# Performance work log

Hardware: AMD Instinct MI355X
Metric: run time of the kernel (lower is better)

The kernel has to match this reference:

```python
import jax, jax.numpy as jnp
import numpy as np

B = 8          # events
P = 16384      # points per event (P > MAX_TOKENS -> selection path)
FEAT = 6
TOK = 768
MT = 128       # max_tokens
K = 16         # k_neighbors
IH = 256       # importance_hidden_dim
LN_EPS = 1e-5


def _linear_init(key, fan_in, fan_out):
    kw, kb = jax.random.split(key)
    lim = 1.0 / np.sqrt(fan_in)
    w = jax.random.uniform(kw, (fan_in, fan_out), jnp.float32, -lim, lim)
    b = jax.random.uniform(kb, (fan_out,), jnp.float32, -lim, lim)
    return w, b


def setup_inputs() -> dict:
    key = jax.random.key(0)
    ks = jax.random.split(key, 16)
    # point data: col0 = batch index (sorted, equal counts), cols1:5 = x,y,z,t
    xyzt = jax.random.normal(ks[0], (B * P, 4), jnp.float32)
    bidx = jnp.repeat(jnp.arange(B, dtype=jnp.float32), P)[:, None]
    coordinates = jnp.concatenate([bidx, xyzt], axis=-1)
    features = jax.random.normal(ks[1], (B * P, FEAT), jnp.float32)
    # gumbel noise = -log(-log(U+1e-10)+1e-10)
    u = jax.random.uniform(ks[2], (B, P), jnp.float32)
    gumbel_noise = -jnp.log(-jnp.log(u + 1e-10) + 1e-10)
    # feature MLP: 6->256->512->768 (ReLU) -> 768
    w1, b1 = _linear_init(ks[3], FEAT, 256)
    w2, b2 = _linear_init(ks[4], 256, 512)
    w3, b3 = _linear_init(ks[5], 512, 768)
    w4, b4 = _linear_init(ks[6], 768, TOK)
    # importance encoder: (768+4)->256, ReLU, LN, 256->256, ReLU, 256->1
    iw1, ib1 = _linear_init(ks[7], TOK + 4, IH)
    ln_g = jnp.ones((IH,), jnp.float32)
    ln_b = jnp.zeros((IH,), jnp.float32)
    iw2, ib2 = _linear_init(ks[8], IH, IH)
    iw3, ib3 = _linear_init(ks[9], IH, 1)
    # neighborhood MLP: 768->768, ReLU, 768->768
    nw1, nb1 = _linear_init(ks[10], TOK, TOK)
    nw2, nb2 = _linear_init(ks[11], TOK, TOK)
    log_temperature = jnp.zeros((), jnp.float32)  # log(1.0)
    return dict(coordinates=coordinates, features=features,
                log_temperature=log_temperature,
                w1=w1, b1=b1, w2=w2, b2=b2, w3=w3, b3=b3, w4=w4, b4=b4,
                iw1=iw1, ib1=ib1, ln_g=ln_g, ln_b=ln_b, iw2=iw2, ib2=ib2,
                iw3=iw3, ib3=ib3, nw1=nw1, nb1=nb1, nw2=nw2, nb2=nb2,
                gumbel_noise=gumbel_noise, batch_size=B)


def _forward(coordinates, features, log_temperature,
             w1, b1, w2, b2, w3, b3, w4, b4,
             iw1, ib1, ln_g, ln_b, iw2, ib2, iw3, ib3,
             nw1, nb1, nw2, nb2, gumbel_noise, batch_size):
    N = coordinates.shape[0]
    Pn = N // batch_size
    coords4 = coordinates[:, 1:5]  # [N,4] (x,y,z,t)
    # point feature MLP
    h = jax.nn.relu(features @ w1 + b1)
    h = jax.nn.relu(h @ w2 + b2)
    h = jax.nn.relu(h @ w3 + b3)
    pf = h @ w4 + b4  # [N, TOK]
    # importance scores (context-aware)
    z = jax.nn.relu(jnp.concatenate([pf, coords4], axis=-1) @ iw1 + ib1)
    mu = jnp.mean(z, axis=-1, keepdims=True)
    var = jnp.var(z, axis=-1, keepdims=True)
    z = (z - mu) / jnp.sqrt(var + LN_EPS) * ln_g + ln_b
    z = jax.nn.relu(z @ iw2 + ib2)
    imp = (z @ iw3 + ib3)[:, 0]  # [N]
    temp = jnp.maximum(jnp.exp(log_temperature), 0.1)
    # equal-count sorted batches -> reshape and vmap over events
    pf_b = pf.reshape(batch_size, Pn, TOK)
    c_b = coords4.reshape(batch_size, Pn, 4)
    imp_b = imp.reshape(batch_size, Pn)

    def per_event(feats, coords, scores, noise):
        # gumbel-softmax top-k selection (soft mode: weights unused downstream)
        pert = (scores + noise) / temp
        _, sel = jax.lax.top_k(pert, MT)            # [MT]
        cent = coords[sel]                           # [MT,4]
        # squared euclidean distances centroids -> all points (same KNN order as cdist)
        d2 = jnp.sum((cent[:, None, :] - coords[None, :, :]) ** 2, axis=-1)  # [MT,P]
        _, knn = jax.lax.top_k(-d2, K)               # [MT,K]
        nbr = feats[knn]                             # [MT,K,TOK]
        pooled = jnp.max(nbr, axis=1)                # [MT,TOK]
        tok = jax.nn.relu(pooled @ nw1 + nb1) @ nw2 + nb2
        order = jnp.argsort(cent[:, 3])              # sort tokens by time
        return tok[order], cent[order]

    tokens, cents = jax.vmap(per_event)(pf_b, c_b, imp_b, gumbel_noise)
    return tokens, cents


def reference(coordinates, features, log_temperature,
              w1, b1, w2, b2, w3, b3, w4, b4,
              iw1, ib1, ln_g, ln_b, iw2, ib2, iw3, ib3,
              nw1, nb1, nw2, nb2, gumbel_noise, batch_size):
    tokens, cents = _forward(coordinates, features, log_temperature,
                             w1, b1, w2, b2, w3, b3, w4, b4,
                             iw1, ib1, ln_g, ln_b, iw2, ib2, iw3, ib3,
                             nw1, nb1, nw2, nb2, gumbel_noise, batch_size)
    masks = jnp.ones((batch_size, MT), dtype=bool)  # all events have > MT points
    return tokens, cents, masks
```

## Files before the change

kernel.cpp:

```cpp
#include <hip/hip_runtime.h>
#include <hip/hip_bf16.h>

#define NPT   131072
#define BATCH 8
#define PPE   16384
#define MT    128
#define KNN   16
#define TOKD  768
#define ZSPLIT 4

typedef short bf16x8 __attribute__((ext_vector_type(8)));
typedef float f32x4  __attribute__((ext_vector_type(4)));

#define GL16(g, l) __builtin_amdgcn_global_load_lds(                         \
    (const __attribute__((address_space(1))) void*)(g),                      \
    (__attribute__((address_space(3))) void*)(l), 16, 0, 0)

__device__ __forceinline__ unsigned pack_hi(unsigned u0, unsigned u1) {
    return (u0 >> 16) | (u1 & 0xFFFF0000u);
}
__device__ __forceinline__ void split1(float x, short& h, short& l) {
    const unsigned u = __float_as_uint(x);
    h = (short)(u >> 16);
    const float r = x - __uint_as_float(u & 0xFFFF0000u);
    l = (short)(__float_as_uint(r) >> 16);
}

__global__ __launch_bounds__(256) void prep_kernel(const float* __restrict__ coords,
                                                   float4* __restrict__ c4f)
{
    const int i = blockIdx.x * 256 + threadIdx.x;
    if (i < NPT) {
        const long b = (long)i * 5;
        c4f[i] = make_float4(coords[b + 1], coords[b + 2], coords[b + 3], coords[b + 4]);
    }
}

__global__ __launch_bounds__(256) void wsplit_all(
    const float* __restrict__ w2, const float* __restrict__ w3,
    const float* __restrict__ w4, const float* __restrict__ iw2,
    const float* __restrict__ nw1, const float* __restrict__ nw2,
    short* w2h, short* w2l, short* w3h, short* w3l,
    short* w4h, short* w4l, short* i2h, short* i2l,
    short* n1h, short* n1l, short* n2h, short* n2l)
{
    const int b = blockIdx.x;
    const float* W; int K, N, Kpad, n; short *hi, *lo;
    if (b < 512)       { W = w2;  K = 256; N = 512; Kpad = 256; hi = w2h; lo = w2l; n = b; }
    else if (b < 1280) { W = w3;  K = 512; N = 768; Kpad = 512; hi = w3h; lo = w3l; n = b - 512; }
    else if (b < 2048) { W = w4;  K = 768; N = 768; Kpad = 768; hi = w4h; lo = w4l; n = b - 1280; }
    else if (b < 2304) { W = iw2; K = 256; N = 256; Kpad = 256; hi = i2h; lo = i2l; n = b - 2048; }
    else if (b < 3072) { W = nw1; K = 768; N = 768; Kpad = 768; hi = n1h; lo = n1l; n = b - 2304; }
    else               { W = nw2; K = 768; N = 768; Kpad = 768; hi = n2h; lo = n2l; n = b - 3072; }
    for (int k = threadIdx.x; k < Kpad; k += 256) {
        short h = 0, l = 0;
        if (k < K) split1(W[(long)k * N + n], h, l);
        hi[(long)n * Kpad + k] = h;
        lo[(long)n * Kpad + k] = l;
    }
}

__global__ __launch_bounds__(256) void w45_kernel(const float* __restrict__ w4,
                                                  const float* __restrict__ iw1,
                                                  const float* __restrict__ b4,
                                                  const float* __restrict__ ib1,
                                                  short* __restrict__ hi,
                                                  short* __restrict__ lo,
                                                  float* __restrict__ bias45)
{
    const int k = blockIdx.x, n = threadIdx.x;
    if (k < 768) {
        const float* wr = w4 + (long)k * 768;
        float v0 = 0.f, v1 = 0.f, v2 = 0.f, v3 = 0.f;
        for (int j = 0; j < 768; j += 4) {
            v0 += wr[j]     * iw1[(long)j * 256 + n];
            v1 += wr[j + 1] * iw1[(long)(j + 1) * 256 + n];
            v2 += wr[j + 2] * iw1[(long)(j + 2) * 256 + n];
            v3 += wr[j + 3] * iw1[(long)(j + 3) * 256 + n];
        }
        const float v = (v0 + v1) + (v2 + v3);
        short h, l; split1(v, h, l);
        hi[(long)n * 800 + k] = h;
        lo[(long)n * 800 + k] = l;
    } else if (k < 800) {
        const float v = (k < 772) ? iw1[(long)k * 256 + n] : 0.f;
        short h, l; split1(v, h, l);
        hi[(long)n * 800 + k] = h;
        lo[(long)n * 800 + k] = l;
    } else {
        float v0 = 0.f, v1 = 0.f, v2 = 0.f, v3 = 0.f;
        for (int j = 0; j < 768; j += 4) {
            v0 += b4[j]     * iw1[(long)j * 256 + n];
            v1 += b4[j + 1] * iw1[(long)(j + 1) * 256 + n];
            v2 += b4[j + 2] * iw1[(long)(j + 2) * 256 + n];
            v3 += b4[j + 3] * iw1[(long)(j + 3) * 256 + n];
        }
        bias45[n] = (v0 + v1) + (v2 + v3) + ib1[n];
    }
}

__global__ __launch_bounds__(256) void l1_kernel(const float* __restrict__ f,
                                                 const float* __restrict__ w1,
                                                 const float* __restrict__ b1,
                                                 short* __restrict__ hp,
                                                 short* __restrict__ lp,
                                                 int base,
                                                 const int* __restrict__ gather)
{
    const int r0 = blockIdx.x << 6, tid = threadIdx.x;
    float wc[6];
#pragma unroll
    for (int k = 0; k < 6; ++k) wc[k] = w1[k * 256 + tid];
    const float bb = b1[tid];
    for (int i = 0; i < 64; ++i) {
        const int r = r0 + i;
        int row = gather ? gather[r] : (base + r);
        row = (row < 0) ? 0 : ((row >= NPT) ? (NPT - 1) : row);
        float acc = bb;
#pragma unroll
        for (int k = 0; k < 6; ++k) acc += f[(long)row * 6 + k] * wc[k];
        acc = fmaxf(acc, 0.f);
        short h, l; split1(acc, h, l);
        hp[(long)r * 256 + tid] = h;
        lp[(long)r * 256 + tid] = l;
    }
}

__global__ __launch_bounds__(256) void gather_h3_kernel(const short* __restrict__ H3,
                                                        const int* __restrict__ knn_idx,
                                                        int off,
                                                        short* __restrict__ G)
{
    const int i = blockIdx.x;
    const int row = knn_idx[off + i];
    const int4* src = (const int4*)(H3 + (long)row * 768);
    int4* dst = (int4*)(G + (long)i * 768);
    if (threadIdx.x < 96) dst[threadIdx.x] = src[threadIdx.x];
}

__global__ __launch_bounds__(256, 3) void gemm_mf(
    const short* __restrict__ Aph, const short* __restrict__ Apl,
    const float* __restrict__ Afp, int Kpad,
    const short* __restrict__ Wth, const short* __restrict__ Wtl,
    const float* __restrict__ bias,
    short* __restrict__ Cph, short* __restrict__ Cpl, int KpadOut,
    float* __restrict__ Cf, short* __restrict__ Cp768,
    float* __restrict__ Cpool,
    const float* __restrict__ CoordC, int cfBase,
    int N, int relu, long partStride)
{
    __shared__ short Ah[128 * 32];
    __shared__ short Al[128 * 32];
    __shared__ short Bh[128 * 32];
    __shared__ short Bl[128 * 32];
    const int tid = threadIdx.x;
    int rowb, colb;
    {
        const int ncol = gridDim.x, nrow = gridDim.y;
        if ((nrow & 7) == 0) {
            const int id  = blockIdx.y * ncol + blockIdx.x;
            const int sgs = ncol << 3;
            const int sg = id / sgs, wi = id % sgs;
            rowb = (sg << 3) + (wi & 7);
            colb = wi >> 3;
        } else { rowb = blockIdx.y; colb = blockIdx.x; }
    }
    const int row0 = rowb << 7, col0 = colb << 7;
    const int wave = tid >> 6, lane = tid & 63;
    const int wr = wave >> 1, wc = wave & 1;
    const int q = lane >> 4, l16 = lane & 15;
    const int l2 = lane >> 2;
    const int ksw = (((lane & 3) ^ ((lane >> 3) & 3)) << 3);
    const int rchunk = ((q ^ ((l16 >> 1) & 3)) << 3);

    f32x4 acc[4][4];
#pragma unroll
    for (int mt = 0; mt < 4; ++mt)
#pragma unroll
        for (int nt = 0; nt < 4; ++nt)
            acc[mt][nt] = (f32x4){0.f, 0.f, 0.f, 0.f};

    const bool useAl = (Apl != nullptr) || (Aph == nullptr);
    const int nkT = Kpad >> 5;
    const int Z = gridDim.z, zb = blockIdx.z;
    const int t0 = (nkT * zb) / Z, t1 = (nkT * (zb + 1)) / Z;

    auto stage = [&](int t) {
        const int k0 = t << 5;
#pragma unroll
        for (int i = 0; i < 2; ++i) {
            const int mb = (wave << 5) + (i << 4);
            const long gb = (long)(col0 + mb + l2) * Kpad + k0 + ksw;
            GL16(&Wth[gb], &Bh[mb * 32]);
            GL16(&Wtl[gb], &Bl[mb * 32]);
        }
        if (Aph) {
#pragma unroll
            for (int i = 0; i < 2; ++i) {
                const int mb = (wave << 5) + (i << 4);
                const long ga = (long)(row0 + mb + l2) * Kpad + k0 + ksw;
                GL16(&Aph[ga], &Ah[mb * 32]);
                if (Apl) GL16(&Apl[ga], &Al[mb * 32]);
            }
        } else {
#pragma unroll
            for (int s = 0; s < 4; ++s) {
                const int l  = (s << 8) + tid;
                const int m  = l >> 3;
                const int k4 = (l & 7) << 2;
                const float4 v = *(const float4*)&Afp[(long)(row0 + m) * Kpad + k0 + k4];
                const unsigned u0 = __float_as_uint(v.x), u1 = __float_as_uint(v.y);
                const unsigned u2 = __float_as_uint(v.z), u3 = __float_as_uint(v.w);
                const unsigned r0 = __float_as_uint(v.x - __uint_as_float(u0 & 0xFFFF0000u));
                const unsigned r1 = __float_as_uint(v.y - __uint_as_float(u1 & 0xFFFF0000u));
                const unsigned r2 = __float_as_uint(v.z - __uint_as_float(u2 & 0xFFFF0000u));
                const unsigned r3 = __float_as_uint(v.w - __uint_as_float(u3 & 0xFFFF0000u));
                const int off = m * 32 + ((((k4 >> 3) ^ ((m >> 1) & 3)) << 3) | (k4 & 4));
                *(int2*)&Ah[off] = make_int2((int)pack_hi(u0, u1), (int)pack_hi(u2, u3));
                *(int2*)&Al[off] = make_int2((int)pack_hi(r0, r1), (int)pack_hi(r2, r3));
            }
        }
    };

    stage(t0);
    __syncthreads();

    for (int t = t0; t < t1; ++t) {
        bf16x8 ah[4], al[4], bh[4], bl[4];
#pragma unroll
        for (int i = 0; i < 4; ++i) {
            const int mrow = (wr << 6) + (i << 4) + l16;
            const int ncol = (wc << 6) + (i << 4) + l16;
            ah[i] = *(const bf16x8*)&Ah[mrow * 32 + rchunk];
            if (useAl) al[i] = *(const bf16x8*)&Al[mrow * 32 + rchunk];
            bh[i] = *(const bf16x8*)&Bh[ncol * 32 + rchunk];
            bl[i] = *(const bf16x8*)&Bl[ncol * 32 + rchunk];
        }
        __syncthreads();
        if (t + 1 < t1) stage(t + 1);
#pragma unroll
        for (int nt = 0; nt < 4; ++nt)
#pragma unroll
            for (int mt = 0; mt < 4; ++mt) {
                acc[mt][nt] = __builtin_amdgcn_mfma_f32_16x16x32_bf16(ah[mt], bh[nt], acc[mt][nt], 0, 0, 0);
                acc[mt][nt] = __builtin_amdgcn_mfma_f32_16x16x32_bf16(ah[mt], bl[nt], acc[mt][nt], 0, 0, 0);
                if (useAl)
                    acc[mt][nt] = __builtin_amdgcn_mfma_f32_16x16x32_bf16(al[mt], bh[nt], acc[mt][nt], 0, 0, 0);
            }
        __syncthreads();
    }

    if (Cf && Z > 1) {
        float* dst = Cf + (long)zb * partStride;
#pragma unroll
        for (int mt = 0; mt < 4; ++mt)
#pragma unroll
            for (int nt = 0; nt < 4; ++nt) {
                const int col = col0 + (wc << 6) + (nt << 4) + l16;
#pragma unroll
                for (int rg = 0; rg < 4; ++rg) {
                    const int row = row0 + (wr << 6) + (mt << 4) + (q << 2) + rg;
                    dst[(long)row * N + col] = acc[mt][nt][rg];
                }
            }
        return;
    }

    if (Cpool) {
#pragma unroll
        for (int mt = 0; mt < 4; ++mt)
#pragma unroll
            for (int nt = 0; nt < 4; ++nt) {
                const int col = col0 + (wc << 6) + (nt << 4) + l16;
                float m = fmaxf(fmaxf(acc[mt][nt][0], acc[mt][nt][1]),
                                fmaxf(acc[mt][nt][2], acc[mt][nt][3]));
                m = fmaxf(m, __shfl_xor(m, 16));
                m = fmaxf(m, __shfl_xor(m, 32));
                m += bias[col];
                if (relu) m = fmaxf(m, 0.f);
                if (q == 0)
                    Cpool[(long)((row0 >> 4) + (wr << 2) + mt) * 768 + col] = m;
            }
        return;
    }
#pragma unroll
    for (int mt = 0; mt < 4; ++mt)
#pragma unroll
        for (int nt = 0; nt < 4; ++nt) {
            const int col = col0 + (wc << 6) + (nt << 4) + l16;
            const float bs = bias[col];
#pragma unroll
            for (int rg = 0; rg < 4; ++rg) {
                const int row = row0 + (wr << 6) + (mt << 4) + (q << 2) + rg;
                float v = acc[mt][nt][rg] + bs;
                if (relu) v = fmaxf(v, 0.f);
                if (Cf) Cf[(long)row * N + col] = v;
                if (Cph || Cp768) {
                    short h, l; split1(v, h, l);
                    if (Cph) {
                        Cph[(long)row * KpadOut + col] = h;
                        Cpl[(long)row * KpadOut + col] = l;
                    }
                    if (Cp768) Cp768[(long)row * 768 + col] = h;
                }
            }
        }
    if (CoordC && Cph && colb == 0 && tid < 128) {
        const int r = row0 + tid;
        const long rb = (long)r * KpadOut;
        const long cb = (long)(cfBase + r) * 5;
#pragma unroll
        for (int d = 0; d < 4; ++d) {
            short h, l; split1(CoordC[cb + 1 + d], h, l);
            Cph[rb + 768 + d] = h;
            Cpl[rb + 768 + d] = l;
        }
        for (int c = 772; c < 800; ++c) { Cph[rb + c] = 0; Cpl[rb + c] = 0; }
    }
}

__global__ __launch_bounds__(256) void ln_kernel(const float* __restrict__ Fp,
                                                 long pstride,
                                                 const float* __restrict__ g,
                                                 const float* __restrict__ b,
                                                 const float* __restrict__ badd,
                                                 short* __restrict__ hp,
                                                 short* __restrict__ lp)
{
    const int tid = threadIdx.x, wave = tid >> 6, lane = tid & 63;
    float gv[4], bv[4], av[4];
#pragma unroll
    for (int j = 0; j < 4; ++j) {
        gv[j] = g[lane * 4 + j]; bv[j] = b[lane * 4 + j]; av[j] = badd[lane * 4 + j];
    }
    for (int i = 0; i < 2; ++i) {
        const int r = (blockIdx.x << 3) + (wave << 1) + i;
        const long off = (long)r * 256 + lane * 4;
        float4 x = *(const float4*)&Fp[off];
#pragma unroll
        for (int z = 1; z < ZSPLIT; ++z) {
            const float4 p = *(const float4*)&Fp[(long)z * pstride + off];
            x.x += p.x; x.y += p.y; x.z += p.z; x.w += p.w;
        }
        x.x = fmaxf(x.x + av[0], 0.f);
        x.y = fmaxf(x.y + av[1], 0.f);
        x.z = fmaxf(x.z + av[2], 0.f);
        x.w = fmaxf(x.w + av[3], 0.f);
        float s = x.x + x.y + x.z + x.w;
#pragma unroll
        for (int off2 = 32; off2; off2 >>= 1) s += __shfl_down(s, off2);
        const float mu = __shfl(s, 0) * (1.f / 256.f);
        const float d0 = x.x - mu, d1 = x.y - mu, d2 = x.z - mu, d3 = x.w - mu;
        float s2 = d0 * d0 + d1 * d1 + d2 * d2 + d3 * d3;
#pragma unroll
        for (int off2 = 32; off2; off2 >>= 1) s2 += __shfl_down(s2, off2);
        const float den = sqrtf(__shfl(s2, 0) * (1.f / 256.f) + 1e-5f);
        const float v[4] = { d0 / den * gv[0] + bv[0], d1 / den * gv[1] + bv[1],
                             d2 / den * gv[2] + bv[2], d3 / den * gv[3] + bv[3] };
#pragma unroll
        for (int j = 0; j < 4; ++j) {
            short h, l; split1(v[j], h, l);
            hp[(long)r * 256 + lane * 4 + j] = h;
            lp[(long)r * 256 + lane * 4 + j] = l;
        }
    }
}

__global__ __launch_bounds__(256) void imp_kernel(const float* __restrict__ Fp,
                                                  long pstride,
                                                  const float* __restrict__ iw3,
                                                  const float* __restrict__ ib3,
                                                  const float* __restrict__ ib2,
                                                  const float* __restrict__ noise,
                                                  const float* __restrict__ lt,
                                                  float* __restrict__ pert,
                                                  int base)
{
    const int tid = threadIdx.x, wave = tid >> 6, lane = tid & 63;
    float wv[4], bv[4];
#pragma unroll
    for (int j = 0; j < 4; ++j) { wv[j] = iw3[lane * 4 + j]; bv[j] = ib2[lane * 4 + j]; }
    const float temp = fmaxf(expf(lt[0]), 0.1f);
    const float b3v = ib3[0];
    for (int i = 0; i < 2; ++i) {
        const int r = (blockIdx.x << 3) + (wave << 1) + i;
        const long off = (long)r * 256 + lane * 4;
        float4 x = *(const float4*)&Fp[off];
#pragma unroll
        for (int z = 1; z < ZSPLIT; ++z) {
            const float4 p = *(const float4*)&Fp[(long)z * pstride + off];
            x.x += p.x; x.y += p.y; x.z += p.z; x.w += p.w;
        }
        float s = fmaxf(x.x + bv[0], 0.f) * wv[0] + fmaxf(x.y + bv[1], 0.f) * wv[1]
                + fmaxf(x.z + bv[2], 0.f) * wv[2] + fmaxf(x.w + bv[3], 0.f) * wv[3];
#pragma unroll
        for (int off2 = 32; off2; off2 >>= 1) s += __shfl_down(s, off2);
        if (lane == 0)
            pert[base + r] = (s + b3v + noise[base + r]) / temp;
    }
}

__device__ __forceinline__ unsigned fmap(float f) {
    unsigned x = __float_as_uint(f);
    return (x & 0x80000000u) ? ~x : (x | 0x80000000u);
}

__global__ __launch_bounds__(256) void topk_kernel(const float* __restrict__ pert,
                                                   const float4* __restrict__ c4f,
                                                   float* __restrict__ centf)
{
    const int e = blockIdx.x, tid = threadIdx.x;
    const int base = e * PPE;
    const int c4 = tid & 3;
    __shared__ unsigned short d16[PPE];
    __shared__ unsigned long long ubuf[664];
    __shared__ int sh_need; __shared__ unsigned sh_b;
    __shared__ int cgt, ceq;
    unsigned* hist4 = (unsigned*)ubuf;
    unsigned* histm = hist4 + 1024;
    for (int i = tid; i < 1024; i += 256) hist4[i] = 0;
    __syncthreads();
    for (int p = tid; p < PPE; p += 256) {
        const unsigned u = fmap(pert[base + p]);
        d16[p] = (unsigned short)(u >> 16);
        atomicAdd(&hist4[((u >> 24) << 2) | c4], 1u);
    }
    __syncthreads();
    histm[tid] = hist4[tid << 2] + hist4[(tid << 2) | 1]
               + hist4[(tid << 2) | 2] + hist4[(tid << 2) | 3];
    __syncthreads();
    if (tid == 0) {
        int cum = 0, b = 255;
        for (; b > 0; --b) { cum += (int)histm[b]; if (cum >= MT) break; }
        if (cum < MT) { cum += (int)histm[0]; b = 0; }
        sh_need = MT - (cum - (int)histm[b]); sh_b = (unsigned)b;
    }
    __syncthreads();
    int need = sh_need;
    const unsigned b1v = sh_b;
    __syncthreads();
    for (int i = tid; i < 1024; i += 256) hist4[i] = 0;
    __syncthreads();
    for (int p = tid; p < PPE; p += 256) {
        const unsigned h = d16[p];
        if ((h >> 8) == b1v) atomicAdd(&hist4[((h & 255u) << 2) | c4], 1u);
    }
    __syncthreads();
    histm[tid] = hist4[tid << 2] + hist4[(tid << 2) | 1]
               + hist4[(tid << 2) | 2] + hist4[(tid << 2) | 3];
    __syncthreads();
    if (tid == 0) {
        int cum = 0, b = 255;
        for (; b > 0; --b) { cum += (int)histm[b]; if (cum >= need) break; }
        if (cum < need) { cum += (int)histm[0]; b = 0; }
        sh_need = need - (cum - (int)histm[b]); sh_b = (unsigned)b;
    }
    __syncthreads();
    need = sh_need;
    const unsigned prefix16 = (b1v << 8) | sh_b;
    int* gt_i = (int*)ubuf;
    unsigned* gt_u = (unsigned*)(gt_i + MT);
    int* eqbuf = (int*)(gt_u + MT);
    unsigned long long* key256 = (unsigned long long*)(eqbuf + 256);
    unsigned long long* key = key256 + 256;
    if (tid == 0) { cgt = 0; ceq = 0; }
    __syncthreads();
    for (int p = tid; p < PPE; p += 256) {
        const unsigned h = d16[p];
        if (h > prefix16)        { int q = atomicAdd(&cgt, 1); if (q < MT)  gt_i[q] = p; }
        else if (h == prefix16)  { int q = atomicAdd(&ceq, 1); if (q < 256) eqbuf[q] = p; }
    }
    __syncthreads();
    const int ngt = (cgt < MT) ? cgt : MT;
    if (tid < ngt) gt_u[tid] = fmap(pert[base + gt_i[tid]]);
    if (ceq <= 256) {
        key256[tid] = (tid < ceq)
            ? (((unsigned long long)fmap(pert[base + eqbuf[tid]]) << 32) | (unsigned)(~eqbuf[tid]))
            : 0ull;
        __syncthreads();
        for (int k = 2; k <= 256; k <<= 1)
            for (int j = k >> 1; j > 0; j >>= 1) {
                const int l = tid ^ j;
                if (l > tid) {
                    const unsigned long long a = key256[tid], b = key256[l];
                    const bool up = ((tid & k) == 0);
                    if (up ? (a < b) : (a > b)) { key256[tid] = b; key256[l] = a; }
                }
                __syncthreads();
            }
    } else if (tid == 0) {
        unsigned long long sel[MT];
        int n = 0;
        for (int p = 0; p < PPE; ++p) {
            if (d16[p] != (unsigned short)prefix16) continue;
            const unsigned long long kk =
                ((unsigned long long)fmap(pert[base + p]) << 32) | (unsigned)(~p);
            if (n < need) {
                int j = n++;
                while (j > 0 && sel[j - 1] < kk) { sel[j] = sel[j - 1]; --j; }
                sel[j] = kk;
            } else if (kk > sel[need - 1]) {
                int j = need - 1;
                while (j > 0 && sel[j - 1] < kk) { sel[j] = sel[j - 1]; --j; }
                sel[j] = kk;
            }
        }
        for (int j = 0; j < need; ++j) key256[j] = sel[j];
    }
    __syncthreads();
    if (tid < MT) {
        if (tid < ngt)
            key[tid] = ((unsigned long long)gt_u[tid] << 32) | (unsigned)(~gt_i[tid]);
        else if (tid < ngt + need)
            key[tid] = key256[tid - ngt];
        else
            key[tid] = 0ull;
    }
    __syncthreads();
    for (int k = 2; k <= MT; k <<= 1)
        for (int j = k >> 1; j > 0; j >>= 1) {
            if (tid < MT) {
                const int l = tid ^ j;
                if (l > tid) {
                    const unsigned long long a = key[tid], b = key[l];
                    const bool up = ((tid & k) == 0);
                    if (up ? (a < b) : (a > b)) { key[tid] = b; key[l] = a; }
                }
            }
            __syncthreads();
        }
    if (tid < MT) {
        const int idx = (int)(~(unsigned)(key[tid] & 0xFFFFFFFFu));
        *(float4*)&centf[(long)(e * MT + tid) * 4] = c4f[base + idx];
    }
}

__device__ __forceinline__ unsigned d2bits(const float4 x, float c0, float c1,
                                           float c2, float c3) {
    const float q0 = __fmul_rn(c0 - x.x, c0 - x.x);
    const float q1 = __fmul_rn(c1 - x.y, c1 - x.y);
    const float q2 = __fmul_rn(c2 - x.z, c2 - x.z);
    const float q3 = __fmul_rn(c3 - x.w, c3 - x.w);
    return __float_as_uint(__fadd_rn(__fadd_rn(__fadd_rn(q0, q1), q2), q3));
}

__global__ __launch_bounds__(256) void knn_kernel(const float4* __restrict__ c4f,
                                                  const float* __restrict__ centf,
                                                  int* __restrict__ knn_idx)
{
    const int blk = blockIdx.x, tid = threadIdx.x;
    const int e = blk >> 7, base = e * PPE;
    const int c4 = tid & 3;
    const float c0 = centf[(long)blk * 4 + 0];
    const float c1 = centf[(long)blk * 4 + 1];
    const float c2 = centf[(long)blk * 4 + 2];
    const float c3 = centf[(long)blk * 4 + 3];
    __shared__ unsigned short d16[PPE];
    __shared__ unsigned long long ubuf[664];
    __shared__ int sh_need; __shared__ unsigned sh_b;
    __shared__ int clt, ceq;
    unsigned* hist4 = (unsigned*)ubuf;
    unsigned* histm = hist4 + 1024;
    for (int i = tid; i < 1024; i += 256) hist4[i] = 0;
    __syncthreads();
    for (int p = tid; p < PPE; p += 256) {
        const unsigned u = d2bits(c4f[base + p], c0, c1, c2, c3);
        d16[p] = (unsigned short)(u >> 16);
        atomicAdd(&hist4[((u >> 24) << 2) | c4], 1u);
    }
    __syncthreads();
    histm[tid] = hist4[tid << 2] + hist4[(tid << 2) | 1]
               + hist4[(tid << 2) | 2] + hist4[(tid << 2) | 3];
    __syncthreads();
    if (tid == 0) {
        int cum = 0, b = 0;
        for (; b < 255; ++b) { cum += (int)histm[b]; if (cum >= KNN) break; }
        if (cum < KNN) { cum += (int)histm[255]; b = 255; }
        sh_need = KNN - (cum - (int)histm[b]); sh_b = (unsigned)b;
    }
    __syncthreads();
    int need = sh_need;
    const unsigned b1v = sh_b;
    __syncthreads();
    for (int i = tid; i < 1024; i += 256) hist4[i] = 0;
    __syncthreads();
    for (int p = tid; p < PPE; p += 256) {
        const unsigned h = d16[p];
        if ((h >> 8) == b1v) atomicAdd(&hist4[((h & 255u) << 2) | c4], 1u);
    }
    __syncthreads();
    histm[tid] = hist4[tid << 2] + hist4[(tid << 2) | 1]
               + hist4[(tid << 2) | 2] + hist4[(tid << 2) | 3];
    __syncthreads();
    if (tid == 0) {
        int cum = 0, b = 0;
        for (; b < 255; ++b) { cum += (int)histm[b]; if (cum >= need) break; }
        if (cum < need) { cum += (int)histm[255]; b = 255; }
        sh_need = need - (cum - (int)histm[b]); sh_b = (unsigned)b;
    }
    __syncthreads();
    need = sh_need;
    const unsigned prefix16 = (b1v << 8) | sh_b;
    int* lt_i = (int*)ubuf;
    unsigned* lt_u = (unsigned*)(lt_i + KNN);
    int* eqbuf = (int*)(lt_u + KNN);
    unsigned long long* key256 = (unsigned long long*)(eqbuf + 256);
    if (tid == 0) { clt = 0; ceq = 0; }
    __syncthreads();
    for (int p = tid; p < PPE; p += 256) {
        const unsigned h = d16[p];
        if (h < prefix16)        { int q = atomicAdd(&clt, 1); if (q < KNN) lt_i[q] = p; }
        else if (h == prefix16)  { int q = atomicAdd(&ceq, 1); if (q < 256) eqbuf[q] = p; }
    }
    __syncthreads();
    const int nlt = (clt < KNN) ? clt : KNN;
    if (tid < nlt) lt_u[tid] = d2bits(c4f[base + lt_i[tid]], c0, c1, c2, c3);
    if (ceq <= 256) {
        key256[tid] = (tid < ceq)
            ? (((unsigned long long)d2bits(c4f[base + eqbuf[tid]], c0, c1, c2, c3) << 32)
               | (unsigned)eqbuf[tid])
            : 0xFFFFFFFFFFFFFFFFull;
        __syncthreads();
        for (int k = 2; k <= 256; k <<= 1)
            for (int j = k >> 1; j > 0; j >>= 1) {
                const int l = tid ^ j;
                if (l > tid) {
                    const unsigned long long a = key256[tid], b = key256[l];
                    const bool up = ((tid & k) == 0);
                    if (up ? (a > b) : (a < b)) { key256[tid] = b; key256[l] = a; }
                }
                __syncthreads();
            }
    } else if (tid == 0) {
        unsigned long long sel[KNN];
        int n = 0;
        for (int p = 0; p < PPE; ++p) {
            if (d16[p] != (unsigned short)prefix16) continue;
            const unsigned long long kk =
                ((unsigned long long)d2bits(c4f[base + p], c0, c1, c2, c3) << 32) | (unsigned)p;
            if (n < need) {
                int j = n++;
                while (j > 0 && sel[j - 1] > kk) { sel[j] = sel[j - 1]; --j; }
                sel[j] = kk;
            } else if (kk < sel[need - 1]) {
                int j = need - 1;
                while (j > 0 && sel[j - 1] > kk) { sel[j] = sel[j - 1]; --j; }
                sel[j] = kk;
            }
        }
        for (int j = 0; j < need; ++j) key256[j] = sel[j];
    }
    __syncthreads();
    if (tid == 0) {
        unsigned long long fin[KNN];
        int n = 0;
        for (int i = 0; i < nlt; ++i) {
            const unsigned long long kk = ((unsigned long long)lt_u[i] << 32) | (unsigned)lt_i[i];
            int j = n++;
            while (j > 0 && fin[j - 1] > kk) { fin[j] = fin[j - 1]; --j; }
            fin[j] = kk;
        }
        for (int i = 0; i < need; ++i) {
            const unsigned long long kk = key256[i];
            int j = n++;
            while (j > 0 && fin[j - 1] > kk) { fin[j] = fin[j - 1]; --j; }
            fin[j] = kk;
        }
        for (int r = 0; r < KNN; ++r)
            knn_idx[blk * KNN + r] = base + (int)(unsigned)(fin[r] & 0xFFFFFFFFu);
    }
}

__global__ __launch_bounds__(256) void emit_kernel(const float* __restrict__ centf,
                                                   const float* __restrict__ tokf,
                                                   float* __restrict__ out,
                                                   long out_size)
{
    const int e = blockIdx.x, s = blockIdx.y, tid = threadIdx.x;
    __shared__ float tv[MT];
    __shared__ int   rk[MT];
    if (tid < MT) tv[tid] = centf[(long)(e * MT + tid) * 4 + 3];
    __syncthreads();
    if (tid < MT) {
        const float t = tv[tid]; int r = 0;
        for (int j = 0; j < MT; ++j)
            r += (tv[j] < t || (tv[j] == t && j < tid)) ? 1 : 0;
        rk[tid] = r;
    }
    __syncthreads();
    const long cent_off = (long)BATCH * MT * TOKD;
    const long mask_off = cent_off + (long)BATCH * MT * 4;
    for (int i = s * 8; i < s * 8 + 8; ++i) {
        const float* src = tokf + ((size_t)e * MT + i) * TOKD;
        const long dst = ((long)e * MT + rk[i]) * TOKD;
        for (int t4 = tid; t4 < TOKD / 4; t4 += 256) {
            const float4 v = ((const float4*)src)[t4];
            const long g = dst + (long)t4 * 4;
            if (g + 3 < out_size) {
                *(float4*)&out[g] = v;
            } else {
                if (g + 0 < out_size) out[g + 0] = v.x;
                if (g + 1 < out_size) out[g + 1] = v.y;
                if (g + 2 < out_size) out[g + 2] = v.z;
                if (g + 3 < out_size) out[g + 3] = v.w;
            }
        }
    }
    if (s == 0) {
        for (int idx = tid; idx < MT * 4; idx += 256) {
            const int i = idx >> 2, d = idx & 3;
            const long g = cent_off + ((long)e * MT + rk[i]) * 4 + d;
            if (g < out_size) out[g] = centf[((long)e * MT + i) * 4 + d];
        }
        for (int idx = tid; idx < MT; idx += 256) {
            const long g = mask_off + (long)e * MT + idx;
            if (g < out_size) out[g] = 1.0f;
        }
    }
}

extern "C" void kernel_launch(void* const* d_in, const int* in_sizes, int n_in,
                              void* d_out, int out_size, void* d_ws, size_t ws_size,
                              hipStream_t stream)
{
    const float* coords = (const float*)d_in[0];
    const float* feats  = (const float*)d_in[1];
    const float* lt     = (const float*)d_in[2];
    const float* w1  = (const float*)d_in[3];  const float* b1  = (const float*)d_in[4];
    const float* w2  = (const float*)d_in[5];  const float* b2  = (const float*)d_in[6];
    const float* w3  = (const float*)d_in[7];  const float* b3  = (const float*)d_in[8];
    const float* w4  = (const float*)d_in[9];  const float* b4  = (const float*)d_in[10];
    const float* iw1 = (const float*)d_in[11]; const float* ib1 = (const float*)d_in[12];
    const float* lng = (const float*)d_in[13]; const float* lnb = (const float*)d_in[14];
    const float* iw2 = (const float*)d_in[15]; const float* ib2 = (const float*)d_in[16];
    const float* iw3 = (const float*)d_in[17]; const float* ib3 = (const float*)d_in[18];
    const float* nw1 = (const float*)d_in[19]; const float* nb1 = (const float*)d_in[20];
    const float* nw2 = (const float*)d_in[21]; const float* nb2 = (const float*)d_in[22];
    const float* noise = (const float*)d_in[23];

    const int NBR = BATCH * MT * KNN;
    const size_t FIXED_FL = (size_t)NPT + 4096 + 16384 + (size_t)1024 * TOKD
                          + (size_t)NPT * 4 + 256 + 2 * (size_t)1024 * TOKD;
    const size_t s_w2 = 512 * 256,  s_w3 = 768 * 512,  s_w4 = 768 * 768;
    const size_t s_45 = 256 * 800,  s_i2 = 256 * 256;
    const size_t s_n1 = 768 * 768,  s_n2 = 768 * 768;
    const size_t WTOT = 2 * (s_w2 + s_w3 + s_w4 + s_45 + s_i2 + s_n1 + s_n2);
    const size_t BASE_BYTES = FIXED_FL * 4 + WTOT * 2;
    const size_t PERROW = (800 * 2 + 512 * 2) * 2 + (size_t)ZSPLIT * 256 * 4;
    int ch = 128;
    while (ch < NPT && BASE_BYTES + (size_t)(ch * 2) * PERROW <= ws_size) ch <<= 1;
    const size_t H3_BYTES = (size_t)NPT * 768 * 2;
    const bool persist = (BASE_BYTES + (size_t)ch * PERROW + H3_BYTES) <= ws_size;

    float*  pert   = (float*)d_ws;
    float*  centf  = pert + NPT;
    int*    knn    = (int*)(centf + 4096);
    float*  pooled = (float*)(knn + 16384);
    float4* c4f    = (float4*)(pooled + (size_t)1024 * TOKD);
    float*  bias45 = (float*)(c4f + NPT);
    float*  T1     = bias45 + 256;
    float*  T2     = T1 + (size_t)1024 * TOKD;
    short*  wsp    = (short*)(T2 + (size_t)1024 * TOKD);
    short* w2h = wsp;            short* w2l = w2h + s_w2;
    short* w3h = w2l + s_w2;     short* w3l = w3h + s_w3;
    short* w4h = w3l + s_w3;     short* w4l = w4h + s_w4;
    short* f45h = w4l + s_w4;    short* f45l = f45h + s_45;
    short* i2h = f45l + s_45;    short* i2l = i2h + s_i2;
    short* n1h = i2l + s_i2;     short* n1l = n1h + s_n1;
    short* n2h = n1l + s_n1;     short* n2l = n2h + s_n2;
    short* PAh = n2l + s_n2;     short* PAl = PAh + (size_t)ch * 800;
    short* PBh = PAl + (size_t)ch * 800;
    short* PBl = PBh + (size_t)ch * 512;
    float* Fp  = (float*)(PBl + (size_t)ch * 512);
    short* H3  = (short*)(Fp + (size_t)ZSPLIT * ch * 256);
    const long pstride = (long)ch * 256;

    prep_kernel<<<dim3((NPT + 255) / 256), dim3(256), 0, stream>>>(coords, c4f);
    wsplit_all<<<dim3(3840), dim3(256), 0, stream>>>(
        w2, w3, w4, iw2, nw1, nw2,
        w2h, w2l, w3h, w3l, w4h, w4l, i2h, i2l, n1h, n1l, n2h, n2l);
    w45_kernel<<<dim3(801), dim3(256), 0, stream>>>(w4, iw1, b4, ib1, f45h, f45l, bias45);

    for (int ck = 0; ck < NPT / ch; ++ck) {
        const int base = ck * ch;
        l1_kernel<<<dim3(ch / 64), dim3(256), 0, stream>>>(feats, w1, b1, PAh, PAl, base, nullptr);
        gemm_mf<<<dim3(512 / 128, ch / 128), dim3(256), 0, stream>>>(
            PAh, PAl, nullptr, 256, w2h, w2l, b2, PBh, PBl, 512,
            nullptr, nullptr, nullptr, nullptr, 0, 512, 1, 0);
        gemm_mf<<<dim3(768 / 128, ch / 128), dim3(256), 0, stream>>>(
            PBh, PBl, nullptr, 512, w3h, w3l, b3, PAh, PAl, 800,
            nullptr, persist ? (H3 + (size_t)base * 768) : nullptr, nullptr,
            coords, base, 768, 1, 0);
        gemm_mf<<<dim3(256 / 128, ch / 128, ZSPLIT), dim3(256), 0, stream>>>(
            PAh, PAl, nullptr, 800, f45h, f45l, nullptr, nullptr, nullptr, 0,
            Fp, nullptr, nullptr, nullptr, 0, 256, 0, pstride);
        ln_kernel<<<dim3(ch / 8), dim3(256), 0, stream>>>(
            Fp, pstride, lng, lnb, bias45, PBh, PBl);
        gemm_mf<<<dim3(256 / 128, ch / 128, ZSPLIT), dim3(256), 0, stream>>>(
            PBh, PBl, nullptr, 256, i2h, i2l, nullptr, nullptr, nullptr, 0,
            Fp, nullptr, nullptr, nullptr, 0, 256, 0, pstride);
        imp_kernel<<<dim3(ch / 8), dim3(256), 0, stream>>>(
            Fp, pstride, iw3, ib3, ib2, noise, lt, pert, base);
    }

    topk_kernel<<<dim3(BATCH), dim3(256), 0, stream>>>(pert, c4f, centf);
    knn_kernel<<<dim3(BATCH * MT), dim3(256), 0, stream>>>(c4f, centf, knn);

    const int rcch = (ch < NBR) ? ch : NBR;
    for (int rc = 0; rc < NBR / rcch; ++rc) {
        if (persist) {
            gather_h3_kernel<<<dim3(rcch), dim3(256), 0, stream>>>(
                H3, knn, rc * rcch, PAh);
            gemm_mf<<<dim3(768 / 128, rcch / 128), dim3(256), 0, stream>>>(
                PAh, nullptr, nullptr, 768, w4h, w4l, b4, nullptr, nullptr, 0,
                nullptr, nullptr, pooled + (size_t)(rc * rcch / 16) * 768,
                nullptr, 0, 768, 0, 0);
        } else {
            l1_kernel<<<dim3(rcch / 64), dim3(256), 0, stream>>>(feats, w1, b1, PAh, PAl, 0, knn + (size_t)rc * rcch);
            gemm_mf<<<dim3(512 / 128, rcch / 128), dim3(256), 0, stream>>>(
                PAh, PAl, nullptr, 256, w2h, w2l, b2, PBh, PBl, 512,
                nullptr, nullptr, nullptr, nullptr, 0, 512, 1, 0);
            gemm_mf<<<dim3(768 / 128, rcch / 128), dim3(256), 0, stream>>>(
                PBh, PBl, nullptr, 512, w3h, w3l, b3, PAh, PAl, 768,
                nullptr, nullptr, nullptr, nullptr, 0, 768, 1, 0);
            gemm_mf<<<dim3(768 / 128, rcch / 128), dim3(256), 0, stream>>>(
                PAh, PAl, nullptr, 768, w4h, w4l, b4, nullptr, nullptr, 0,
                nullptr, nullptr, pooled + (size_t)(rc * rcch / 16) * 768,
                nullptr, 0, 768, 0, 0);
        }
    }

    gemm_mf<<<dim3(768 / 128, 1024 / 128), dim3(256), 0, stream>>>(
        nullptr, nullptr, pooled, 768, n1h, n1l, nb1, nullptr, nullptr, 0,
        T1, nullptr, nullptr, nullptr, 0, 768, 1, 0);
    gemm_mf<<<dim3(768 / 128, 1024 / 128), dim3(256), 0, stream>>>(
        nullptr, nullptr, T1, 768, n2h, n2l, nb2, nullptr, nullptr, 0,
        T2, nullptr, nullptr, nullptr, 0, 768, 0, 0);
    emit_kernel<<<dim3(BATCH, 16), dim3(256), 0, stream>>>(
        centf, T2, (float*)d_out, (long)out_size);
}
```

Measured before the change: 1.875 ms.

## Replace single-block radix top-k with two-stage bitonic partial sort and merge

The per-event radix-histogram top-k, which ran on only 8 blocks, is replaced by a two-stage scheme. 64 blocks each bitonic-sort a 2048-element slice and emit their top 128 candidates, then 8 merge blocks sort the 1024 candidates per event. This spreads the selection across more CUs at the cost of more sorting work, an extra launch and a candidate buffer. ZSPLIT also drops from 4 to 2, halving the split-K partial buffers and the reduction work in the LN and importance kernels in exchange for less parallelism in those GEMMs.

Result: faster. 1.673 ms (-10.8%).

```diff
diff --git a/kernel.cpp b/kernel.cpp
--- a/kernel.cpp
+++ b/kernel.cpp
@@ -7,7 +7,7 @@
 #define MT    128
 #define KNN   16
 #define TOKD  768
-#define ZSPLIT 4
+#define ZSPLIT 2
 
 typedef short bf16x8 __attribute__((ext_vector_type(8)));
 typedef float f32x4  __attribute__((ext_vector_type(4)));
@@ -405,133 +405,54 @@
     return (x & 0x80000000u) ? ~x : (x | 0x80000000u);
 }
 
-__global__ __launch_bounds__(256) void topk_kernel(const float* __restrict__ pert,
-                                                   const float4* __restrict__ c4f,
-                                                   float* __restrict__ centf)
+__global__ __launch_bounds__(256) void topk_part(const float* __restrict__ pert,
+                                                 unsigned long long* __restrict__ cand)
+{
+    const int e = blockIdx.x >> 3, s = blockIdx.x & 7, tid = threadIdx.x;
+    const int base = e * PPE + s * 2048;
+    __shared__ unsigned long long key[2048];
+    for (int i = tid; i < 2048; i += 256)
+        key[i] = ((unsigned long long)fmap(pert[base + i]) << 32) | (unsigned)(~(base + i));
+    __syncthreads();
+    for (int k = 2; k <= 2048; k <<= 1)
+        for (int j = k >> 1; j > 0; j >>= 1) {
+            for (int i = tid; i < 2048; i += 256) {
+                const int l = i ^ j;
+                if (l > i) {
+                    const unsigned long long a = key[i], b = key[l];
+                    const bool up = ((i & k) == 0);
+                    if (up ? (a < b) : (a > b)) { key[i] = b; key[l] = a; }
+                }
+            }
+            __syncthreads();
+        }
+    if (tid < MT) cand[(long)blockIdx.x * MT + tid] = key[tid];
+}
+
+__global__ __launch_bounds__(256) void topk_merge(const unsigned long long* __restrict__ cand,
+                                                  const float4* __restrict__ c4f,
+                                                  float* __restrict__ centf)
 {
     const int e = blockIdx.x, tid = threadIdx.x;
-    const int base = e * PPE;
-    const int c4 = tid & 3;
-    __shared__ unsigned short d16[PPE];
-    __shared__ unsigned long long ubuf[664];
-    __shared__ int sh_need; __shared__ unsigned sh_b;
-    __shared__ int cgt, ceq;
-    unsigned* hist4 = (unsigned*)ubuf;
-    unsigned* histm = hist4 + 1024;
-    for (int i = tid; i < 1024; i += 256) hist4[i] = 0;
-    __syncthreads();
-    for (int p = tid; p < PPE; p += 256) {
-        const unsigned u = fmap(pert[base + p]);
-        d16[p] = (unsigned short)(u >> 16);
-        atomicAdd(&hist4[((u >> 24) << 2) | c4], 1u);
-    }
-    __syncthreads();
-    histm[tid] = hist4[tid << 2] + hist4[(tid << 2) | 1]
-               + hist4[(tid << 2) | 2] + hist4[(tid << 2) | 3];
-    __syncthreads();
-    if (tid == 0) {
-        int cum = 0, b = 255;
-        for (; b > 0; --b) { cum += (int)histm[b]; if (cum >= MT) break; }
-        if (cum < MT) { cum += (int)histm[0]; b = 0; }
-        sh_need = MT - (cum - (int)histm[b]); sh_b = (unsigned)b;
-    }
-    __syncthreads();
-    int need = sh_need;
-    const unsigned b1v = sh_b;
-    __syncthreads();
-    for (int i = tid; i < 1024; i += 256) hist4[i] = 0;
-    __syncthreads();
-    for (int p = tid; p < PPE; p += 256) {
-        const unsigned h = d16[p];
-        if ((h >> 8) == b1v) atomicAdd(&hist4[((h & 255u) << 2) | c4], 1u);
-    }
-    __syncthreads();
-    histm[tid] = hist4[tid << 2] + hist4[(tid << 2) | 1]
-               + hist4[(tid << 2) | 2] + hist4[(tid << 2) | 3];
-    __syncthreads();
-    if (tid == 0) {
-        int cum = 0, b = 255;
-        for (; b > 0; --b) { cum += (int)histm[b]; if (cum >= need) break; }
-        if (cum < need) { cum += (int)histm[0]; b = 0; }
-        sh_need = need - (cum - (int)histm[b]); sh_b = (unsigned)b;
-    }
-    __syncthreads();
-    need = sh_need;
-    const unsigned prefix16 = (b1v << 8) | sh_b;
-    int* gt_i = (int*)ubuf;
-    unsigned* gt_u = (unsigned*)(gt_i + MT);
-    int* eqbuf = (int*)(gt_u + MT);
-    unsigned long long* key256 = (unsigned long long*)(eqbuf + 256);
-    unsigned long long* key = key256 + 256;
-    if (tid == 0) { cgt = 0; ceq = 0; }
-    __syncthreads();
-    for (int p = tid; p < PPE; p += 256) {
-        const unsigned h = d16[p];
-        if (h > prefix16)        { int q = atomicAdd(&cgt, 1); if (q < MT)  gt_i[q] = p; }
-        else if (h == prefix16)  { int q = atomicAdd(&ceq, 1); if (q < 256) eqbuf[q] = p; }
-    }
-    __syncthreads();
-    const int ngt = (cgt < MT) ? cgt : MT;
-    if (tid < ngt) gt_u[tid] = fmap(pert[base + gt_i[tid]]);
-    if (ceq <= 256) {
-        key256[tid] = (tid < ceq)
-            ? (((unsigned long long)fmap(pert[base + eqbuf[tid]]) << 32) | (unsigned)(~eqbuf[tid]))
-            : 0ull;
-        __syncthreads();
-        for (int k = 2; k <= 256; k <<= 1)
-            for (int j = k >> 1; j > 0; j >>= 1) {
-                const int l = tid ^ j;
-                if (l > tid) {
-                    const unsigned long long a = key256[tid], b = key256[l];
-                    const bool up = ((tid & k) == 0);
-                    if (up ? (a < b) : (a > b)) { key256[tid] = b; key256[l] = a; }
-                }
-                __syncthreads();
-            }
-    } else if (tid == 0) {
-        unsigned long long sel[MT];
-        int n = 0;
-        for (int p = 0; p < PPE; ++p) {
-            if (d16[p] != (unsigned short)prefix16) continue;
-            const unsigned long long kk =
-                ((unsigned long long)fmap(pert[base + p]) << 32) | (unsigned)(~p);
-            if (n < need) {
-                int j = n++;
-                while (j > 0 && sel[j - 1] < kk) { sel[j] = sel[j - 1]; --j; }
-                sel[j] = kk;
-            } else if (kk > sel[need - 1]) {
-                int j = need - 1;
-                while (j > 0 && sel[j - 1] < kk) { sel[j] = sel[j - 1]; --j; }
-                sel[j] = kk;
-            }
-        }
-        for (int j = 0; j < need; ++j) key256[j] = sel[j];
-    }
-    __syncthreads();
-    if (tid < MT) {
-        if (tid < ngt)
-            key[tid] = ((unsigned long long)gt_u[tid] << 32) | (unsigned)(~gt_i[tid]);
-        else if (tid < ngt + need)
-            key[tid] = key256[tid - ngt];
-        else
-            key[tid] = 0ull;
-    }
-    __syncthreads();
-    for (int k = 2; k <= MT; k <<= 1)
+    __shared__ unsigned long long key[1024];
+    for (int i = tid; i < 1024; i += 256)
+        key[i] = cand[(long)e * 1024 + i];
+    __syncthreads();
+    for (int k = 2; k <= 1024; k <<= 1)
         for (int j = k >> 1; j > 0; j >>= 1) {
-            if (tid < MT) {
-                const int l = tid ^ j;
-                if (l > tid) {
-                    const unsigned long long a = key[tid], b = key[l];
-                    const bool up = ((tid & k) == 0);
-                    if (up ? (a < b) : (a > b)) { key[tid] = b; key[l] = a; }
+            for (int i = tid; i < 1024; i += 256) {
+                const int l = i ^ j;
+                if (l > i) {
+                    const unsigned long long a = key[i], b = key[l];
+                    const bool up = ((i & k) == 0);
+                    if (up ? (a < b) : (a > b)) { key[i] = b; key[l] = a; }
                 }
             }
             __syncthreads();
         }
     if (tid < MT) {
         const int idx = (int)(~(unsigned)(key[tid] & 0xFFFFFFFFu));
-        *(float4*)&centf[(long)(e * MT + tid) * 4] = c4f[base + idx];
+        *(float4*)&centf[(long)(e * MT + tid) * 4] = c4f[idx];
     }
 }
 
@@ -739,7 +660,7 @@
     const float* noise = (const float*)d_in[23];
 
     const int NBR = BATCH * MT * KNN;
-    const size_t FIXED_FL = (size_t)NPT + 4096 + 16384 + (size_t)1024 * TOKD
+    const size_t FIXED_FL = (size_t)NPT + 4096 + 16384 + 16384 + (size_t)1024 * TOKD
                           + (size_t)NPT * 4 + 256 + 2 * (size_t)1024 * TOKD;
     const size_t s_w2 = 512 * 256,  s_w3 = 768 * 512,  s_w4 = 768 * 768;
     const size_t s_45 = 256 * 800,  s_i2 = 256 * 256;
@@ -755,7 +676,8 @@
     float*  pert   = (float*)d_ws;
     float*  centf  = pert + NPT;
     int*    knn    = (int*)(centf + 4096);
-    float*  pooled = (float*)(knn + 16384);
+    unsigned long long* cand = (unsigned long long*)(knn + 16384);
+    float*  pooled = (float*)(cand + 8192);
     float4* c4f    = (float4*)(pooled + (size_t)1024 * TOKD);
     float*  bias45 = (float*)(c4f + NPT);
     float*  T1     = bias45 + 256;
@@ -803,7 +725,8 @@
             Fp, pstride, iw3, ib3, ib2, noise, lt, pert, base);
     }
 
-    topk_kernel<<<dim3(BATCH), dim3(256), 0, stream>>>(pert, c4f, centf);
+    topk_part<<<dim3(BATCH * 8), dim3(256), 0, stream>>>(pert, cand);
+    topk_merge<<<dim3(BATCH), dim3(256), 0, stream>>>(cand, c4f, centf);
     knn_kernel<<<dim3(BATCH * MT), dim3(256), 0, stream>>>(c4f, centf, knn);
 
     const int rcch = (ch < NBR) ? ch : NBR;
```
